# Kernel optimization log

Measured on AMD Instinct MI355X. Metric: run time of the kernel, lower is better.

The kernel has to match this reference:

```python
import jax, jax.numpy as jnp
import numpy as np

B, S, D, H = 2, 2048, 1024, 16
DH = D // H
CAUSAL = True


def setup_inputs() -> dict:
    key = jax.random.key(0)
    ks = jax.random.split(key, 11)
    s = 1.0 / np.sqrt(D)
    return {
        "x": jax.random.normal(ks[0], (B, S, D), dtype=jnp.float32),
        "Wq": jax.random.uniform(ks[1], (D, D), jnp.float32, -s, s),
        "bq": jax.random.uniform(ks[2], (D,), jnp.float32, -s, s),
        "Wk": jax.random.uniform(ks[3], (D, D), jnp.float32, -s, s),
        "bk": jax.random.uniform(ks[4], (D,), jnp.float32, -s, s),
        "Wv": jax.random.uniform(ks[5], (D, D), jnp.float32, -s, s),
        "bv": jax.random.uniform(ks[6], (D,), jnp.float32, -s, s),
        "Wo": jax.random.uniform(ks[7], (D, D), jnp.float32, -s, s),
        "bo": jax.random.uniform(ks[8], (D,), jnp.float32, -s, s),
        "ln_g": jnp.ones((D,), jnp.float32),
        "ln_b": jnp.zeros((D,), jnp.float32),
    }


def reference(x, Wq, bq, Wk, bk, Wv, bv, Wo, bo, ln_g, ln_b):
    scale = np.sqrt(DH).astype(np.float32)
    # projections -> [B, H, S, DH]
    def proj(W, b):
        return (x @ W.T + b).reshape(B, S, H, DH).transpose(0, 2, 1, 3)
    Q, K, V = proj(Wq, bq), proj(Wk, bk), proj(Wv, bv)
    scores = jnp.einsum("bhsd,bhtd->bhst", Q, K) / scale  # [B,H,S,S]
    if CAUSAL:
        causal = jnp.tril(jnp.ones((S, S), dtype=bool))
        scores = jnp.where(causal, scores, -jnp.inf)
    attn = jax.nn.softmax(scores, axis=-1)
    ctx = jnp.einsum("bhst,bhtd->bhsd", attn, V)
    ctx = ctx.transpose(0, 2, 1, 3).reshape(B, S, D)
    attn_out = ctx @ Wo.T + bo
    y = x + attn_out
    mu = jnp.mean(y, axis=-1, keepdims=True)
    var = jnp.mean(jnp.square(y - mu), axis=-1, keepdims=True)
    return (y - mu) / jnp.sqrt(var + 1e-5) * ln_g + ln_b
```

## Files before the change

### kernel.cpp

```cpp
#include <hip/hip_runtime.h>
#include <stdint.h>

#define B_   2
#define S_   2048
#define D_   1024
#define H_   16
#define DH_  64
#define MTOK (B_*S_)

typedef __attribute__((ext_vector_type(8))) short  short8v;
typedef __attribute__((ext_vector_type(4))) float  f32x4;
typedef __attribute__((ext_vector_type(16))) float f32x16;
typedef __attribute__((ext_vector_type(4))) unsigned int uint4v;

__device__ __forceinline__ unsigned short f2bf(float f) {
  unsigned int u = __builtin_bit_cast(unsigned int, f);
  unsigned int r = (u + 0x7fffu + ((u >> 16) & 1u)) >> 16;
  return (unsigned short)r;
}

__device__ __forceinline__ f32x4 zero4() { f32x4 v = {0.f, 0.f, 0.f, 0.f}; return v; }
__device__ __forceinline__ f32x16 zero16() {
  f32x16 v;
#pragma unroll
  for (int i = 0; i < 16; ++i) v[i] = 0.f;
  return v;
}

__device__ __forceinline__ unsigned int cvtpk(float lo, float hi) {
  unsigned int d;
  asm("v_cvt_pk_bf16_f32 %0, %1, %2" : "=v"(d) : "v"(lo), "v"(hi));
  return d;
}
__device__ __forceinline__ void plswap(unsigned int& a, unsigned int& b) {
  asm("v_permlane32_swap_b32 %0, %1" : "+v"(a), "+v"(b));
}

__device__ __forceinline__ void gload16(const void* g, void* l) {
  __builtin_amdgcn_global_load_lds(
      (const __attribute__((address_space(1))) void*)g,
      (__attribute__((address_space(3))) void*)l, 16, 0, 0);
}

__global__ void cvt_all_kernel(
    const float* __restrict__ x,
    const float* __restrict__ w0, const float* __restrict__ w1,
    const float* __restrict__ w2, const float* __restrict__ w3,
    unsigned short* __restrict__ xb,
    unsigned short* __restrict__ o0, unsigned short* __restrict__ o1,
    unsigned short* __restrict__ o2, unsigned short* __restrict__ o3)
{
  int i = blockIdx.x * blockDim.x + threadIdx.x;
  const float* in;
  unsigned short* out;
  int off;
  if (i < MTOK * D_ / 4) {
    in = x; out = xb; off = i;
  } else {
    int j = i - MTOK * D_ / 4;
    int w = j >> 18;
    off = j & 262143;
    in  = (w == 0) ? w0 : (w == 1) ? w1 : (w == 2) ? w2 : w3;
    out = (w == 0) ? o0 : (w == 1) ? o1 : (w == 2) ? o2 : o3;
  }
  float4 v = reinterpret_cast<const float4*>(in)[off];
  ushort4 o;
  o.x = f2bf(v.x); o.y = f2bf(v.y); o.z = f2bf(v.z); o.w = f2bf(v.w);
  reinterpret_cast<ushort4*>(out)[off] = o;
}

__device__ __forceinline__ void stage_gemm32(
    const unsigned short* __restrict__ A, const unsigned short* __restrict__ Bt,
    int K, int m0, int n0, int k0, unsigned short* As, unsigned short* Bs, int tid)
{
#pragma unroll
  for (int it = 0; it < 2; ++it) {
    int fa = it * 256 + tid;
    int row = fa >> 2, slot = fa & 3;
    int gs = slot ^ (row & 3);
    gload16(A + (size_t)(m0 + row) * K + k0 + gs * 8, (char*)As + fa * 16);
  }
#pragma unroll
  for (int it = 0; it < 2; ++it) {
    int fa = it * 256 + tid;
    int row = fa >> 2, slot = fa & 3;
    int gs = slot ^ (row & 3);
    gload16(Bt + (size_t)(n0 + row) * K + k0 + gs * 8, (char*)Bs + fa * 16);
  }
}

__device__ __forceinline__ void gemm_mainloop(
    const unsigned short* __restrict__ A, const unsigned short* __restrict__ Bt,
    int K, int m0, int n0, unsigned short* As, unsigned short* Bs, f32x4 acc[4][4])
{
  const int tid = threadIdx.x;
  const int lane = tid & 63, wid = tid >> 6;
  const int wr = wid >> 1, wc = wid & 1;
  const int l15 = lane & 15, g = lane >> 4;

#pragma unroll
  for (int mi = 0; mi < 4; ++mi)
#pragma unroll
    for (int ni = 0; ni < 4; ++ni) acc[mi][ni] = zero4();

  const int nk = K >> 5;
  stage_gemm32(A, Bt, K, m0, n0, 0, As, Bs, tid);
  asm volatile("s_waitcnt vmcnt(0)" ::: "memory");
  __builtin_amdgcn_s_barrier();
  asm volatile("" ::: "memory");

  for (int k = 0; k < nk; ++k) {
    if (k + 1 < nk)
      stage_gemm32(A, Bt, K, m0, n0, (k + 1) << 5,
                   As + ((k + 1) & 1) * 4096, Bs + ((k + 1) & 1) * 4096, tid);
    const char* Ab = (const char*)(As + (k & 1) * 4096);
    const char* Bb = (const char*)(Bs + (k & 1) * 4096);
    short8v af[4], bfr[4];
#pragma unroll
    for (int mi = 0; mi < 4; ++mi) {
      int row = wr * 64 + mi * 16 + l15;
      int slot = g ^ (row & 3);
      af[mi] = *(const short8v*)(Ab + row * 64 + slot * 16);
    }
#pragma unroll
    for (int ni = 0; ni < 4; ++ni) {
      int row = wc * 64 + ni * 16 + l15;
      int slot = g ^ (row & 3);
      bfr[ni] = *(const short8v*)(Bb + row * 64 + slot * 16);
    }
#pragma unroll
    for (int mi = 0; mi < 4; ++mi)
#pragma unroll
      for (int ni = 0; ni < 4; ++ni)
        acc[mi][ni] = __builtin_amdgcn_mfma_f32_16x16x32_bf16(af[mi], bfr[ni], acc[mi][ni], 0, 0, 0);
    asm volatile("s_waitcnt vmcnt(0)" ::: "memory");
    __builtin_amdgcn_s_barrier();
    asm volatile("" ::: "memory");
  }
}

__global__ __launch_bounds__(256) void gemm_qkv_kernel(
    const unsigned short* __restrict__ xb,
    const unsigned short* __restrict__ wqb, const unsigned short* __restrict__ wkb,
    const unsigned short* __restrict__ wvb,
    const float* __restrict__ bq, const float* __restrict__ bk, const float* __restrict__ bv,
    unsigned short* __restrict__ Qb, unsigned short* __restrict__ Kb, unsigned short* __restrict__ VTb)
{
  __shared__ __align__(16) unsigned short As[2 * 128 * 32];
  __shared__ __align__(16) unsigned short Bs[2 * 128 * 32];
  const int z = blockIdx.z;
  const unsigned short* Bt = (z == 0) ? wqb : (z == 1) ? wkb : wvb;
  const float* bias = (z == 0) ? bq : (z == 1) ? bk : bv;
  const float scl = (z == 0) ? 0.180336880f : 1.0f;
  const int m0 = blockIdx.y * 128, n0 = blockIdx.x * 128;

  f32x4 acc[4][4];
  gemm_mainloop(xb, Bt, D_, m0, n0, As, Bs, acc);

  const int tid = threadIdx.x, lane = tid & 63, wid = tid >> 6;
  const int wr = wid >> 1, wc = wid & 1, l15 = lane & 15, g = lane >> 4;
#pragma unroll
  for (int ni = 0; ni < 4; ++ni) {
    int n = n0 + wc * 64 + ni * 16 + l15;
    float bia = bias[n];
    int hh = n >> 6, dh = n & 63;
#pragma unroll
    for (int mi = 0; mi < 4; ++mi) {
      int mbase = m0 + wr * 64 + mi * 16 + 4 * g;
      int b = mbase >> 11;
      int s0 = mbase & 2047;
      if (z < 2) {
        unsigned short* o = (z == 0) ? Qb : Kb;
#pragma unroll
        for (int r = 0; r < 4; ++r) {
          float v = (acc[mi][ni][r] + bia) * scl;
          o[(((size_t)(b * H_ + hh) * S_ + (s0 + r)) << 6) + dh] = f2bf(v);
        }
      } else {
        ushort4 o;
        o.x = f2bf(acc[mi][ni][0] + bia);
        o.y = f2bf(acc[mi][ni][1] + bia);
        o.z = f2bf(acc[mi][ni][2] + bia);
        o.w = f2bf(acc[mi][ni][3] + bia);
        *(ushort4*)(VTb + ((size_t)(b * H_ + hh) * DH_ + dh) * S_ + s0) = o;
      }
    }
  }
}

__device__ __forceinline__ void stage_tile128(
    const unsigned short* Kh, const unsigned short* Vh, int t0, char* base, int tid)
{
#pragma unroll
  for (int it = 0; it < 4; ++it) {
    int fa = it * 256 + tid;
    int row = fa >> 3, slot = fa & 7, gs = slot ^ (row & 7);
    gload16(Kh + (size_t)(t0 + row) * DH_ + gs * 8, base + fa * 16);
  }
#pragma unroll
  for (int it = 0; it < 4; ++it) {
    int fa = it * 256 + tid;
    int row = fa >> 4, slot = fa & 15;
    int gs = slot ^ (row & 7);
    gload16(Vh + (size_t)row * S_ + t0 + gs * 8, base + 16384 + fa * 16);
  }
}

__global__ __launch_bounds__(256, 2) void attn_kernel(
    const unsigned short* __restrict__ Qb, const unsigned short* __restrict__ Kb,
    const unsigned short* __restrict__ VTb, unsigned short* __restrict__ ctxb)
{
  __shared__ __align__(16) char smem[65536];
  const int tid = threadIdx.x, lane = tid & 63, wid = tid >> 6;
  const int l31 = lane & 31, h = lane >> 5;
  const int fid = blockIdx.x;
  const int bh = (fid & 7) * 4 + ((fid >> 3) & 3);
  const int qpos = fid >> 5;
  const int qi = (qpos < 8) ? qpos : 23 - qpos;
  const int qblk = qi * 128;
  const int q0w = qblk + wid * 32;
  const int qg = q0w + l31;
  const unsigned short* Qh = Qb + (size_t)bh * S_ * DH_;
  const unsigned short* Kh = Kb + (size_t)bh * S_ * DH_;
  const unsigned short* Vh = VTb + (size_t)bh * DH_ * S_;

  short8v qf[4];
#pragma unroll
  for (int kk = 0; kk < 4; ++kk)
    qf[kk] = *(const short8v*)(Qh + (size_t)qg * DH_ + kk * 16 + h * 8);

  f32x16 ctx0 = zero16(), ctx1 = zero16();
  float mrun = -3e38f, lrun = 0.f;

  const int ntm1 = qi;
  stage_tile128(Kh, Vh, 0, smem, tid);
  asm volatile("s_waitcnt vmcnt(0)" ::: "memory");
  __builtin_amdgcn_s_barrier();
  asm volatile("" ::: "memory");

  for (int t = 0; t <= ntm1; ++t) {
    if (t < ntm1) stage_tile128(Kh, Vh, (t + 1) << 7, smem + (((t + 1) & 1) * 32768), tid);
    const char* Kbuf = smem + (t & 1) * 32768;
    const char* Vbuf = Kbuf + 16384;
#pragma unroll
    for (int sub = 0; sub < 2; ++sub) {
      const int t0 = (t << 7) + (sub << 6);
      if (t0 <= q0w + 31) {
        const char* Kt = Kbuf + sub * 8192;

        f32x16 s0 = zero16(), s1 = zero16();
        __builtin_amdgcn_s_setprio(1);
#pragma unroll
        for (int kk = 0; kk < 4; ++kk) {
          int slot = (2 * kk + h) ^ (l31 & 7);
          short8v kf0 = *(const short8v*)(Kt + l31 * 128 + slot * 16);
          short8v kf1 = *(const short8v*)(Kt + (32 + l31) * 128 + slot * 16);
          s0 = __builtin_amdgcn_mfma_f32_32x32x16_bf16(kf0, qf[kk], s0, 0, 0, 0);
          s1 = __builtin_amdgcn_mfma_f32_32x32x16_bf16(kf1, qf[kk], s1, 0, 0, 0);
        }
        __builtin_amdgcn_s_setprio(0);
        if (t0 + 63 > q0w) {
#pragma unroll
          for (int r = 0; r < 16; ++r) {
            int k0i = (r & 3) + 8 * (r >> 2) + 4 * h;
            if (t0 + k0i > qg) s0[r] = -1e30f;
            if (t0 + k0i + 32 > qg) s1[r] = -1e30f;
          }
        }
        float tm;
        {
          float m01[8];
#pragma unroll
          for (int r = 0; r < 8; ++r)
            m01[r] = fmaxf(fmaxf(s0[r], s0[r + 8]), fmaxf(s1[r], s1[r + 8]));
          float a = fmaxf(fmaxf(m01[0], m01[1]), fmaxf(m01[2], m01[3]));
          float b = fmaxf(fmaxf(m01[4], m01[5]), fmaxf(m01[6], m01[7]));
          tm = fmaxf(a, b);
        }
        tm = fmaxf(tm, __shfl_xor(tm, 32));

        if (!__all(tm <= mrun + 8.f)) {
          float mnew = fmaxf(mrun, tm);
          float al = exp2f(mrun - mnew);
#pragma unroll
          for (int r = 0; r < 16; ++r) { ctx0[r] *= al; ctx1[r] *= al; }
          lrun *= al;
          mrun = mnew;
        }
        float p[32];
        float psa0 = 0.f, psa1 = 0.f, psa2 = 0.f, psa3 = 0.f;
#pragma unroll
        for (int r = 0; r < 16; r += 4) {
          p[r + 0] = exp2f(s0[r + 0] - mrun); psa0 += p[r + 0];
          p[r + 1] = exp2f(s0[r + 1] - mrun); psa1 += p[r + 1];
          p[r + 2] = exp2f(s0[r + 2] - mrun); psa2 += p[r + 2];
          p[r + 3] = exp2f(s0[r + 3] - mrun); psa3 += p[r + 3];
        }
#pragma unroll
        for (int r = 0; r < 16; r += 4) {
          p[16 + r + 0] = exp2f(s1[r + 0] - mrun); psa0 += p[16 + r + 0];
          p[16 + r + 1] = exp2f(s1[r + 1] - mrun); psa1 += p[16 + r + 1];
          p[16 + r + 2] = exp2f(s1[r + 2] - mrun); psa2 += p[16 + r + 2];
          p[16 + r + 3] = exp2f(s1[r + 3] - mrun); psa3 += p[16 + r + 3];
        }
        float ps = (psa0 + psa1) + (psa2 + psa3);
        ps += __shfl_xor(ps, 32);
        lrun += ps;

        unsigned int pk[16];
#pragma unroll
        for (int m = 0; m < 16; ++m) pk[m] = cvtpk(p[2 * m], p[2 * m + 1]);
#pragma unroll
        for (int base = 0; base < 16; base += 4) {
          plswap(pk[base + 0], pk[base + 2]);
          plswap(pk[base + 1], pk[base + 3]);
        }
        __builtin_amdgcn_s_setprio(1);
#pragma unroll
        for (int dt = 0; dt < 2; ++dt) {
          int row = dt * 32 + l31;
#pragma unroll
          for (int kt = 0; kt < 4; ++kt) {
            int slot = (2 * kt + h) ^ (row & 7);
            short8v vf = *(const short8v*)(Vbuf + row * 256 + sub * 128 + slot * 16);
            uint4v u = {pk[4 * kt], pk[4 * kt + 1], pk[4 * kt + 2], pk[4 * kt + 3]};
            short8v pf = __builtin_bit_cast(short8v, u);
            if (dt == 0) ctx0 = __builtin_amdgcn_mfma_f32_32x32x16_bf16(vf, pf, ctx0, 0, 0, 0);
            else         ctx1 = __builtin_amdgcn_mfma_f32_32x32x16_bf16(vf, pf, ctx1, 0, 0, 0);
          }
        }
        __builtin_amdgcn_s_setprio(0);
      }
    }
    asm volatile("s_waitcnt vmcnt(0)" ::: "memory");
    __builtin_amdgcn_s_barrier();
    asm volatile("" ::: "memory");
  }

  float cf[32];
#pragma unroll
  for (int r = 0; r < 16; ++r) { cf[r] = ctx0[r]; cf[16 + r] = ctx1[r]; }
  const int b = bh >> 4, hcol = (bh & 15) * 64;
  unsigned short* orow = ctxb + (((size_t)(b * S_ + qg)) << 10) + hcol;
  float invL = 1.0f / lrun;
#pragma unroll
  for (int j = 0; j < 8; ++j) {
    uint2 w;
    w.x = cvtpk(cf[4 * j + 0] * invL, cf[4 * j + 1] * invL);
    w.y = cvtpk(cf[4 * j + 2] * invL, cf[4 * j + 3] * invL);
    *(uint2*)(orow + 32 * (j >> 2) + 8 * (j & 3) + 4 * h) = w;
  }
}

__global__ __launch_bounds__(256) void gemm_out_kernel(
    const unsigned short* __restrict__ ctxb, const unsigned short* __restrict__ wob,
    const float* __restrict__ bo, const float* __restrict__ x, float* __restrict__ y)
{
  __shared__ __align__(16) unsigned short As[2 * 128 * 32];
  __shared__ __align__(16) unsigned short Bs[2 * 128 * 32];
  const int m0 = blockIdx.y * 128, n0 = blockIdx.x * 128;
  f32x4 acc[4][4];
  gemm_mainloop(ctxb, wob, D_, m0, n0, As, Bs, acc);

  const int tid = threadIdx.x, lane = tid & 63, wid = tid >> 6;
  const int wr = wid >> 1, wc = wid & 1, l15 = lane & 15, g = lane >> 4;
#pragma unroll
  for (int ni = 0; ni < 4; ++ni) {
    int n = n0 + wc * 64 + ni * 16 + l15;
    float bia = bo[n];
#pragma unroll
    for (int mi = 0; mi < 4; ++mi) {
      int mbase = m0 + wr * 64 + mi * 16 + 4 * g;
#pragma unroll
      for (int r = 0; r < 4; ++r) {
        size_t idx = ((size_t)(mbase + r) << 10) + n;
        y[idx] = acc[mi][ni][r] + bia + x[idx];
      }
    }
  }
}

__global__ __launch_bounds__(256) void ln_kernel(
    float* __restrict__ y, const float* __restrict__ gw, const float* __restrict__ bw)
{
  const int row = blockIdx.x;
  float* p = y + ((size_t)row << 10);
  const int t = threadIdx.x;
  float4 v = *(const float4*)(p + t * 4);
  float s  = v.x + v.y + v.z + v.w;
  float s2 = v.x * v.x + v.y * v.y + v.z * v.z + v.w * v.w;
#pragma unroll
  for (int d = 1; d < 64; d <<= 1) { s += __shfl_xor(s, d); s2 += __shfl_xor(s2, d); }
  __shared__ float ps[4], ps2[4];
  const int lane = t & 63, wid = t >> 6;
  if (lane == 0) { ps[wid] = s; ps2[wid] = s2; }
  __syncthreads();
  s  = ps[0] + ps[1] + ps[2] + ps[3];
  s2 = ps2[0] + ps2[1] + ps2[2] + ps2[3];
  float mu  = s * (1.f / 1024.f);
  float var = s2 * (1.f / 1024.f) - mu * mu;
  float rstd = rsqrtf(var + 1e-5f);
  float4 gv = *(const float4*)(gw + t * 4);
  float4 bv = *(const float4*)(bw + t * 4);
  float4 o;
  o.x = (v.x - mu) * rstd * gv.x + bv.x;
  o.y = (v.y - mu) * rstd * gv.y + bv.y;
  o.z = (v.z - mu) * rstd * gv.z + bv.z;
  o.w = (v.w - mu) * rstd * gv.w + bv.w;
  *(float4*)(p + t * 4) = o;
}

extern "C" void kernel_launch(void* const* d_in, const int* in_sizes, int n_in,
                              void* d_out, int out_size, void* d_ws, size_t ws_size,
                              hipStream_t stream) {
  const float* x   = (const float*)d_in[0];
  const float* Wq  = (const float*)d_in[1];
  const float* bq  = (const float*)d_in[2];
  const float* Wk  = (const float*)d_in[3];
  const float* bk  = (const float*)d_in[4];
  const float* Wv  = (const float*)d_in[5];
  const float* bv  = (const float*)d_in[6];
  const float* Wo  = (const float*)d_in[7];
  const float* bo  = (const float*)d_in[8];
  const float* lng = (const float*)d_in[9];
  const float* lnb = (const float*)d_in[10];
  float* out = (float*)d_out;

  char* ws = (char*)d_ws;
  unsigned short* xb  = (unsigned short*)ws;                 ws += (size_t)MTOK * D_ * 2;
  unsigned short* wqb = (unsigned short*)ws;                 ws += (size_t)D_ * D_ * 2;
  unsigned short* wkb = (unsigned short*)ws;                 ws += (size_t)D_ * D_ * 2;
  unsigned short* wvb = (unsigned short*)ws;                 ws += (size_t)D_ * D_ * 2;
  unsigned short* wob = (unsigned short*)ws;                 ws += (size_t)D_ * D_ * 2;
  unsigned short* Qb  = (unsigned short*)ws;                 ws += (size_t)B_ * H_ * S_ * DH_ * 2;
  unsigned short* Kb  = (unsigned short*)ws;                 ws += (size_t)B_ * H_ * S_ * DH_ * 2;
  unsigned short* VTb = (unsigned short*)ws;                 ws += (size_t)B_ * H_ * DH_ * S_ * 2;
  unsigned short* ctxb = (unsigned short*)ws;                ws += (size_t)MTOK * D_ * 2;

  cvt_all_kernel<<<(MTOK * D_ / 4 + 4 * D_ * D_ / 4) / 256, 256, 0, stream>>>(
      x, Wq, Wk, Wv, Wo, xb, wqb, wkb, wvb, wob);

  gemm_qkv_kernel<<<dim3(D_ / 128, MTOK / 128, 3), 256, 0, stream>>>(
      xb, wqb, wkb, wvb, bq, bk, bv, Qb, Kb, VTb);

  attn_kernel<<<dim3((S_ / 128) * B_ * H_), 256, 0, stream>>>(Qb, Kb, VTb, ctxb);

  gemm_out_kernel<<<dim3(D_ / 128, MTOK / 128), 256, 0, stream>>>(ctxb, wob, bo, x, out);

  ln_kernel<<<MTOK, 256, 0, stream>>>(out, lng, lnb);
}
```

Measured before the change: 136.4 us.

## Split attention KV range across two wave groups per block with LSE merge

The attention kernel now runs 512 threads per block, with two groups of four waves each handling alternate 128-key tiles for the same 128 query rows. Both tiles are staged per step into a 128 KB double-buffered LDS region. At the end, partial max, sum and context are merged through shared memory using a log-sum-exp combine. This aims to halve the serial KV loop length per block and improve latency hiding. The cost is lower occupancy (one block per CU, 128 KB LDS), an extra merge pass, and idle waves when the tile count is odd.

```diff
diff --git a/kernel.cpp b/kernel.cpp
--- a/kernel.cpp
+++ b/kernel.cpp
@@ -188,37 +188,38 @@
   }
 }
 
-__device__ __forceinline__ void stage_tile128(
+__device__ __forceinline__ void stage_tile128_w8(
     const unsigned short* Kh, const unsigned short* Vh, int t0, char* base, int tid)
 {
 #pragma unroll
-  for (int it = 0; it < 4; ++it) {
-    int fa = it * 256 + tid;
+  for (int it = 0; it < 2; ++it) {
+    int fa = it * 512 + tid;
     int row = fa >> 3, slot = fa & 7, gs = slot ^ (row & 7);
     gload16(Kh + (size_t)(t0 + row) * DH_ + gs * 8, base + fa * 16);
   }
 #pragma unroll
-  for (int it = 0; it < 4; ++it) {
-    int fa = it * 256 + tid;
+  for (int it = 0; it < 2; ++it) {
+    int fa = it * 512 + tid;
     int row = fa >> 4, slot = fa & 15;
     int gs = slot ^ (row & 7);
     gload16(Vh + (size_t)row * S_ + t0 + gs * 8, base + 16384 + fa * 16);
   }
 }
 
-__global__ __launch_bounds__(256, 2) void attn_kernel(
+__global__ __launch_bounds__(512, 1) void attn_kernel(
     const unsigned short* __restrict__ Qb, const unsigned short* __restrict__ Kb,
     const unsigned short* __restrict__ VTb, unsigned short* __restrict__ ctxb)
 {
-  __shared__ __align__(16) char smem[65536];
+  __shared__ __align__(16) char smem[131072];
   const int tid = threadIdx.x, lane = tid & 63, wid = tid >> 6;
+  const int qw = wid & 3, kp = wid >> 2;
   const int l31 = lane & 31, h = lane >> 5;
   const int fid = blockIdx.x;
   const int bh = (fid & 7) * 4 + ((fid >> 3) & 3);
   const int qpos = fid >> 5;
   const int qi = (qpos < 8) ? qpos : 23 - qpos;
   const int qblk = qi * 128;
-  const int q0w = qblk + wid * 32;
+  const int q0w = qblk + qw * 32;
   const int qg = q0w + l31;
   const unsigned short* Qh = Qb + (size_t)bh * S_ * DH_;
   const unsigned short* Kh = Kb + (size_t)bh * S_ * DH_;
@@ -232,104 +233,115 @@
   f32x16 ctx0 = zero16(), ctx1 = zero16();
   float mrun = -3e38f, lrun = 0.f;
 
-  const int ntm1 = qi;
-  stage_tile128(Kh, Vh, 0, smem, tid);
+  const int nt = qi + 1;
+  const int ns = (nt + 1) >> 1;
+
+  stage_tile128_w8(Kh, Vh, 0, smem, tid);
+  if (nt > 1) stage_tile128_w8(Kh, Vh, 128, smem + 32768, tid);
   asm volatile("s_waitcnt vmcnt(0)" ::: "memory");
   __builtin_amdgcn_s_barrier();
   asm volatile("" ::: "memory");
 
-  for (int t = 0; t <= ntm1; ++t) {
-    if (t < ntm1) stage_tile128(Kh, Vh, (t + 1) << 7, smem + (((t + 1) & 1) * 32768), tid);
-    const char* Kbuf = smem + (t & 1) * 32768;
-    const char* Vbuf = Kbuf + 16384;
-#pragma unroll
-    for (int sub = 0; sub < 2; ++sub) {
-      const int t0 = (t << 7) + (sub << 6);
-      if (t0 <= q0w + 31) {
-        const char* Kt = Kbuf + sub * 8192;
-
-        f32x16 s0 = zero16(), s1 = zero16();
-        __builtin_amdgcn_s_setprio(1);
-#pragma unroll
-        for (int kk = 0; kk < 4; ++kk) {
-          int slot = (2 * kk + h) ^ (l31 & 7);
-          short8v kf0 = *(const short8v*)(Kt + l31 * 128 + slot * 16);
-          short8v kf1 = *(const short8v*)(Kt + (32 + l31) * 128 + slot * 16);
-          s0 = __builtin_amdgcn_mfma_f32_32x32x16_bf16(kf0, qf[kk], s0, 0, 0, 0);
-          s1 = __builtin_amdgcn_mfma_f32_32x32x16_bf16(kf1, qf[kk], s1, 0, 0, 0);
+  for (int s = 0; s < ns; ++s) {
+    if (s + 1 < ns) {
+      int u0 = 2 * (s + 1);
+      char* nb = smem + ((s + 1) & 1) * 65536;
+      stage_tile128_w8(Kh, Vh, u0 << 7, nb, tid);
+      if (u0 + 1 < nt) stage_tile128_w8(Kh, Vh, (u0 + 1) << 7, nb + 32768, tid);
+    }
+    const int t = 2 * s + kp;
+    if (t < nt) {
+      const char* Kbuf = smem + (s & 1) * 65536 + kp * 32768;
+      const char* Vbuf = Kbuf + 16384;
+#pragma unroll
+      for (int sub = 0; sub < 2; ++sub) {
+        const int t0 = (t << 7) + (sub << 6);
+        if (t0 <= q0w + 31) {
+          const char* Kt = Kbuf + sub * 8192;
+
+          f32x16 s0 = zero16(), s1 = zero16();
+          __builtin_amdgcn_s_setprio(1);
+#pragma unroll
+          for (int kk = 0; kk < 4; ++kk) {
+            int slot = (2 * kk + h) ^ (l31 & 7);
+            short8v kf0 = *(const short8v*)(Kt + l31 * 128 + slot * 16);
+            short8v kf1 = *(const short8v*)(Kt + (32 + l31) * 128 + slot * 16);
+            s0 = __builtin_amdgcn_mfma_f32_32x32x16_bf16(kf0, qf[kk], s0, 0, 0, 0);
+            s1 = __builtin_amdgcn_mfma_f32_32x32x16_bf16(kf1, qf[kk], s1, 0, 0, 0);
+          }
+          __builtin_amdgcn_s_setprio(0);
+          if (t0 + 63 > q0w) {
+#pragma unroll
+            for (int r = 0; r < 16; ++r) {
+              int k0i = (r & 3) + 8 * (r >> 2) + 4 * h;
+              if (t0 + k0i > qg) s0[r] = -1e30f;
+              if (t0 + k0i + 32 > qg) s1[r] = -1e30f;
+            }
+          }
+          float tm;
+          {
+            float m01[8];
+#pragma unroll
+            for (int r = 0; r < 8; ++r)
+              m01[r] = fmaxf(fmaxf(s0[r], s0[r + 8]), fmaxf(s1[r], s1[r + 8]));
+            float a = fmaxf(fmaxf(m01[0], m01[1]), fmaxf(m01[2], m01[3]));
+            float b = fmaxf(fmaxf(m01[4], m01[5]), fmaxf(m01[6], m01[7]));
+            tm = fmaxf(a, b);
+          }
+          tm = fmaxf(tm, __shfl_xor(tm, 32));
+
+          if (!__all(tm <= mrun + 8.f)) {
+            float mnew = fmaxf(mrun, tm);
+            float al = exp2f(mrun - mnew);
+#pragma unroll
+            for (int r = 0; r < 16; ++r) { ctx0[r] *= al; ctx1[r] *= al; }
+            lrun *= al;
+            mrun = mnew;
+          }
+          float p[32];
+          float psa0 = 0.f, psa1 = 0.f, psa2 = 0.f, psa3 = 0.f;
+#pragma unroll
+          for (int r = 0; r < 16; r += 4) {
+            p[r + 0] = exp2f(s0[r + 0] - mrun); psa0 += p[r + 0];
+            p[r + 1] = exp2f(s0[r + 1] - mrun); psa1 += p[r + 1];
+            p[r + 2] = exp2f(s0[r + 2] - mrun); psa2 += p[r + 2];
+            p[r + 3] = exp2f(s0[r + 3] - mrun); psa3 += p[r + 3];
+          }
+#pragma unroll
+          for (int r = 0; r < 16; r += 4) {
+            p[16 + r + 0] = exp2f(s1[r + 0] - mrun); psa0 += p[16 + r + 0];
+            p[16 + r + 1] = exp2f(s1[r + 1] - mrun); psa1 += p[16 + r + 1];
+            p[16 + r + 2] = exp2f(s1[r + 2] - mrun); psa2 += p[16 + r + 2];
+            p[16 + r + 3] = exp2f(s1[r + 3] - mrun); psa3 += p[16 + r + 3];
+          }
+          float ps = (psa0 + psa1) + (psa2 + psa3);
+          ps += __shfl_xor(ps, 32);
+          lrun += ps;
+
+          unsigned int pk[16];
+#pragma unroll
+          for (int m = 0; m < 16; ++m) pk[m] = cvtpk(p[2 * m], p[2 * m + 1]);
+#pragma unroll
+          for (int base = 0; base < 16; base += 4) {
+            plswap(pk[base + 0], pk[base + 2]);
+            plswap(pk[base + 1], pk[base + 3]);
+          }
+          __builtin_amdgcn_s_setprio(1);
+#pragma unroll
+          for (int dt = 0; dt < 2; ++dt) {
+            int row = dt * 32 + l31;
+#pragma unroll
+            for (int kt = 0; kt < 4; ++kt) {
+              int slot = (2 * kt + h) ^ (row & 7);
+              short8v vf = *(const short8v*)(Vbuf + row * 256 + sub * 128 + slot * 16);
+              uint4v u = {pk[4 * kt], pk[4 * kt + 1], pk[4 * kt + 2], pk[4 * kt + 3]};
+              short8v pf = __builtin_bit_cast(short8v, u);
+              if (dt == 0) ctx0 = __builtin_amdgcn_mfma_f32_32x32x16_bf16(vf, pf, ctx0, 0, 0, 0);
+              else         ctx1 = __builtin_amdgcn_mfma_f32_32x32x16_bf16(vf, pf, ctx1, 0, 0, 0);
+            }
+          }
+          __builtin_amdgcn_s_setprio(0);
         }
-        __builtin_amdgcn_s_setprio(0);
-        if (t0 + 63 > q0w) {
-#pragma unroll
-          for (int r = 0; r < 16; ++r) {
-            int k0i = (r & 3) + 8 * (r >> 2) + 4 * h;
-            if (t0 + k0i > qg) s0[r] = -1e30f;
-            if (t0 + k0i + 32 > qg) s1[r] = -1e30f;
-          }
-        }
-        float tm;
-        {
-          float m01[8];
-#pragma unroll
-          for (int r = 0; r < 8; ++r)
-            m01[r] = fmaxf(fmaxf(s0[r], s0[r + 8]), fmaxf(s1[r], s1[r + 8]));
-          float a = fmaxf(fmaxf(m01[0], m01[1]), fmaxf(m01[2], m01[3]));
-          float b = fmaxf(fmaxf(m01[4], m01[5]), fmaxf(m01[6], m01[7]));
-          tm = fmaxf(a, b);
-        }
-        tm = fmaxf(tm, __shfl_xor(tm, 32));
-
-        if (!__all(tm <= mrun + 8.f)) {
-          float mnew = fmaxf(mrun, tm);
-          float al = exp2f(mrun - mnew);
-#pragma unroll
-          for (int r = 0; r < 16; ++r) { ctx0[r] *= al; ctx1[r] *= al; }
-          lrun *= al;
-          mrun = mnew;
-        }
-        float p[32];
-        float psa0 = 0.f, psa1 = 0.f, psa2 = 0.f, psa3 = 0.f;
-#pragma unroll
-        for (int r = 0; r < 16; r += 4) {
-          p[r + 0] = exp2f(s0[r + 0] - mrun); psa0 += p[r + 0];
-          p[r + 1] = exp2f(s0[r + 1] - mrun); psa1 += p[r + 1];
-          p[r + 2] = exp2f(s0[r + 2] - mrun); psa2 += p[r + 2];
-          p[r + 3] = exp2f(s0[r + 3] - mrun); psa3 += p[r + 3];
-        }
-#pragma unroll
-        for (int r = 0; r < 16; r += 4) {
-          p[16 + r + 0] = exp2f(s1[r + 0] - mrun); psa0 += p[16 + r + 0];
-          p[16 + r + 1] = exp2f(s1[r + 1] - mrun); psa1 += p[16 + r + 1];
-          p[16 + r + 2] = exp2f(s1[r + 2] - mrun); psa2 += p[16 + r + 2];
-          p[16 + r + 3] = exp2f(s1[r + 3] - mrun); psa3 += p[16 + r + 3];
-        }
-        float ps = (psa0 + psa1) + (psa2 + psa3);
-        ps += __shfl_xor(ps, 32);
-        lrun += ps;
-
-        unsigned int pk[16];
-#pragma unroll
-        for (int m = 0; m < 16; ++m) pk[m] = cvtpk(p[2 * m], p[2 * m + 1]);
-#pragma unroll
-        for (int base = 0; base < 16; base += 4) {
-          plswap(pk[base + 0], pk[base + 2]);
-          plswap(pk[base + 1], pk[base + 3]);
-        }
-        __builtin_amdgcn_s_setprio(1);
-#pragma unroll
-        for (int dt = 0; dt < 2; ++dt) {
-          int row = dt * 32 + l31;
-#pragma unroll
-          for (int kt = 0; kt < 4; ++kt) {
-            int slot = (2 * kt + h) ^ (row & 7);
-            short8v vf = *(const short8v*)(Vbuf + row * 256 + sub * 128 + slot * 16);
-            uint4v u = {pk[4 * kt], pk[4 * kt + 1], pk[4 * kt + 2], pk[4 * kt + 3]};
-            short8v pf = __builtin_bit_cast(short8v, u);
-            if (dt == 0) ctx0 = __builtin_amdgcn_mfma_f32_32x32x16_bf16(vf, pf, ctx0, 0, 0, 0);
-            else         ctx1 = __builtin_amdgcn_mfma_f32_32x32x16_bf16(vf, pf, ctx1, 0, 0, 0);
-          }
-        }
-        __builtin_amdgcn_s_setprio(0);
       }
     }
     asm volatile("s_waitcnt vmcnt(0)" ::: "memory");
@@ -337,18 +349,38 @@
     asm volatile("" ::: "memory");
   }
 
-  float cf[32];
-#pragma unroll
-  for (int r = 0; r < 16; ++r) { cf[r] = ctx0[r]; cf[16 + r] = ctx1[r]; }
-  const int b = bh >> 4, hcol = (bh & 15) * 64;
-  unsigned short* orow = ctxb + (((size_t)(b * S_ + qg)) << 10) + hcol;
-  float invL = 1.0f / lrun;
-#pragma unroll
-  for (int j = 0; j < 8; ++j) {
-    uint2 w;
-    w.x = cvtpk(cf[4 * j + 0] * invL, cf[4 * j + 1] * invL);
-    w.y = cvtpk(cf[4 * j + 2] * invL, cf[4 * j + 3] * invL);
-    *(uint2*)(orow + 32 * (j >> 2) + 8 * (j & 3) + 4 * h) = w;
+  float* cws = (float*)smem + qw * 2176;
+  if (kp == 1) {
+#pragma unroll
+    for (int r = 0; r < 16; ++r) {
+      cws[r * 64 + lane]        = ctx0[r];
+      cws[(16 + r) * 64 + lane] = ctx1[r];
+    }
+    cws[32 * 64 + lane] = mrun;
+    cws[33 * 64 + lane] = lrun;
+  }
+  __syncthreads();
+  if (kp == 0) {
+    float pm = cws[32 * 64 + lane], pl = cws[33 * 64 + lane];
+    float m  = fmaxf(mrun, pm);
+    float sa = exp2f(mrun - m), sb = exp2f(pm - m);
+    float L  = lrun * sa + pl * sb;
+    float cf[32];
+#pragma unroll
+    for (int r = 0; r < 16; ++r) {
+      cf[r]      = ctx0[r] * sa + cws[r * 64 + lane] * sb;
+      cf[16 + r] = ctx1[r] * sa + cws[(16 + r) * 64 + lane] * sb;
+    }
+    const int b = bh >> 4, hcol = (bh & 15) * 64;
+    unsigned short* orow = ctxb + (((size_t)(b * S_ + qg)) << 10) + hcol;
+    float invL = 1.0f / L;
+#pragma unroll
+    for (int j = 0; j < 8; ++j) {
+      uint2 w;
+      w.x = cvtpk(cf[4 * j + 0] * invL, cf[4 * j + 1] * invL);
+      w.y = cvtpk(cf[4 * j + 2] * invL, cf[4 * j + 3] * invL);
+      *(uint2*)(orow + 32 * (j >> 2) + 8 * (j & 3) + 4 * h) = w;
+    }
   }
 }
 
@@ -443,7 +475,7 @@
   gemm_qkv_kernel<<<dim3(D_ / 128, MTOK / 128, 3), 256, 0, stream>>>(
       xb, wqb, wkb, wvb, bq, bk, bv, Qb, Kb, VTb);
 
-  attn_kernel<<<dim3((S_ / 128) * B_ * H_), 256, 0, stream>>>(Qb, Kb, VTb, ctxb);
+  attn_kernel<<<dim3((S_ / 128) * B_ * H_), 512, 0, stream>>>(Qb, Kb, VTb, ctxb);
 
   gemm_out_kernel<<<dim3(D_ / 128, MTOK / 128), 256, 0, stream>>>(ctxb, wob, bo, x, out);
 
```

Measured after the change: 131.8 us. 3.4% less time.
